# Kernel optimization log

Hardware: AMD Instinct MI355X
Metric: run time of the kernel (lower is better)

Reference implementation:

```python
import jax, jax.numpy as jnp
import numpy as np

S, L = 4096, 16          # words per sentence, max chars per word
V, DW, DC, H, T = 128000, 128, 64, 256, 50
CHAR_VOCAB = 53


def lstm_cell(h, c, x, Wih, Whh, bih, bhh):
    # PyTorch LSTM gate order: i, f, g, o
    g = x @ Wih.T + h @ Whh.T + bih + bhh
    i, f, gg, o = jnp.split(g, 4, axis=-1)
    c = jax.nn.sigmoid(f) * c + jax.nn.sigmoid(i) * jnp.tanh(gg)
    h = jax.nn.sigmoid(o) * jnp.tanh(c)
    return h, c


def setup_inputs() -> dict:
    key = jax.random.key(0)
    ks = jax.random.split(key, 14)
    s = 0.1
    return {
        "word_ids": jax.random.randint(ks[0], (S,), 0, V),
        "char_ids": jax.random.randint(ks[1], (S, L), 0, CHAR_VOCAB),
        "word_lengths": jax.random.randint(ks[2], (S,), 1, L + 1),
        "word_emb": jax.random.normal(ks[3], (V, DW), jnp.float32) * s,
        "char_emb": jax.random.normal(ks[4], (CHAR_VOCAB, DC), jnp.float32) * s,
        "c_Wih": jax.random.normal(ks[5], (4 * DC, DC), jnp.float32) * s,
        "c_Whh": jax.random.normal(ks[6], (4 * DC, DC), jnp.float32) * s,
        "c_bih": jnp.zeros((4 * DC,), jnp.float32),
        "c_bhh": jnp.zeros((4 * DC,), jnp.float32),
        "w_Wih": jax.random.normal(ks[7], (4 * H, DW + DC), jnp.float32) * s,
        "w_Whh": jax.random.normal(ks[8], (4 * H, H), jnp.float32) * s,
        "w_bih": jnp.zeros((4 * H,), jnp.float32),
        "w_bhh": jnp.zeros((4 * H,), jnp.float32),
        "out_W": jax.random.normal(ks[9], (T, H), jnp.float32) * s,
        "out_b": jnp.zeros((T,), jnp.float32),
    }


def reference(word_ids, char_ids, word_lengths, word_emb, char_emb,
              c_Wih, c_Whh, c_bih, c_bhh,
              w_Wih, w_Whh, w_bih, w_bhh, out_W, out_b):
    # --- char-level LSTM, all words batched together, masked for ragged lengths ---
    ce = char_emb[char_ids]                 # [S, L, DC]
    xs = jnp.swapaxes(ce, 0, 1)             # [L, S, DC]

    def char_step(carry, inp):
        h, c = carry
        x, t = inp
        hn, cn = lstm_cell(h, c, x, c_Wih, c_Whh, c_bih, c_bhh)
        valid = (t < word_lengths)[:, None]  # freeze state once past word length
        return (jnp.where(valid, hn, h), jnp.where(valid, cn, c)), None

    z = jnp.zeros((S, DC), ce.dtype)
    (h_char, _), _ = jax.lax.scan(char_step, (z, z), (xs, jnp.arange(L)))

    # --- word-level LSTM over the sentence (batch = 1, as in the original) ---
    we = word_emb[word_ids]                          # [S, DW]
    wx = jnp.concatenate([we, h_char], axis=-1)      # [S, DW+DC]

    def word_step(carry, x):
        h, c = lstm_cell(carry[0], carry[1], x, w_Wih, w_Whh, w_bih, w_bhh)
        return (h, c), h

    zh = jnp.zeros((H,), wx.dtype)
    _, hs = jax.lax.scan(word_step, (zh, zh), wx)    # hs: [S, H]

    logits = hs @ out_W.T + out_b                    # [S, T]
    return jax.nn.log_softmax(logits, axis=1)
```

## Files before the change

### kernel.cpp

```cpp
#include <hip/hip_runtime.h>
#include <hip/hip_bf16.h>
#include <math.h>

#define S   4096
#define L   16
#define DW  128
#define DC  64
#define HH  256
#define TT  50
#define KX  (DW + DC)
#define G4  (4 * HH)
#define CWPG 8
#define SB  16

typedef unsigned long long u64;

__device__ __forceinline__ float frcp(float x) { return __builtin_amdgcn_rcpf(x); }
__device__ __forceinline__ float fsigmoid(float x) { return frcp(1.f + __expf(-x)); }
__device__ __forceinline__ float ftanh(float x) {
    float ax = fabsf(x);
    float t  = __expf(-2.f * ax);
    float r  = (1.f - t) * frcp(1.f + t);
    return x < 0.f ? -r : r;
}

__device__ __forceinline__ void publish_h(u64* p, int tag, float v) {
    u64 pk = ((u64)(unsigned)tag << 32) | (u64)__float_as_uint(v);
    __hip_atomic_store(p, pk, __ATOMIC_RELAXED, __HIP_MEMORY_SCOPE_AGENT);
}
__device__ __forceinline__ float poll_h(const u64* p, int tag) {
    u64 v;
    do {
        v = __hip_atomic_load(p, __ATOMIC_RELAXED, __HIP_MEMORY_SCOPE_AGENT);
    } while ((int)(unsigned)(v >> 32) != tag);
    return __uint_as_float((unsigned)v);
}

__global__ __launch_bounds__(256) void char_lstm_kernel(
    const int* __restrict__ char_ids, const int* __restrict__ word_len,
    const float* __restrict__ char_emb,
    const float* __restrict__ cWih, const float* __restrict__ cWhh,
    const float* __restrict__ cbih, const float* __restrict__ cbhh,
    float* __restrict__ h_char)
{
    const int t = threadIdx.x;
    const int g = t >> 6;
    const int j = t & 63;
    const int r = g * 64 + j;

    float wih[64], whh[64];
#pragma unroll
    for (int k = 0; k < 64; ++k) wih[k] = cWih[r * 64 + k];
#pragma unroll
    for (int k = 0; k < 64; ++k) whh[k] = cWhh[r * 64 + k];
    const float cb = cbih[r] + cbhh[r];

    __shared__ float ce[L * 64];
    __shared__ float hbuf[64];
    __shared__ float gbuf[256];
    __shared__ int   ids[L];
    __shared__ int   wlen;

    const int w0 = blockIdx.x * CWPG;
    for (int wi = 0; wi < CWPG; ++wi) {
        const int w = w0 + wi;
        if (t < L)   ids[t] = char_ids[w * L + t];
        if (t == 64) wlen = word_len[w];
        if (t < 64)  hbuf[t] = 0.f;
        float c = 0.f;
        float hreg = 0.f;
        __syncthreads();
        for (int i = t; i < L * 64; i += 256)
            ce[i] = char_emb[ids[i >> 6] * 64 + (i & 63)];
        __syncthreads();

        for (int step = 0; step < L; ++step) {
            float acc = cb;
            const float* x = &ce[step * 64];
#pragma unroll
            for (int k = 0; k < 64; k += 4) {
                float4 xv = *(const float4*)&x[k];
                acc += wih[k] * xv.x + wih[k + 1] * xv.y + wih[k + 2] * xv.z + wih[k + 3] * xv.w;
            }
#pragma unroll
            for (int k = 0; k < 64; k += 4) {
                float4 hv = *(const float4*)&hbuf[k];
                acc += whh[k] * hv.x + whh[k + 1] * hv.y + whh[k + 2] * hv.z + whh[k + 3] * hv.w;
            }
            float a = (g == 2) ? ftanh(acc) : fsigmoid(acc);
            gbuf[r] = a;
            __syncthreads();
            if (g == 0) {
                if (step < wlen) {
                    float iv = gbuf[j], fv = gbuf[64 + j], gg = gbuf[128 + j], ov = gbuf[192 + j];
                    c = fv * c + iv * gg;
                    hreg = ov * ftanh(c);
                }
                hbuf[j] = hreg;
            }
            __syncthreads();
        }
        if (g == 0) h_char[w * 64 + j] = hreg;
        __syncthreads();
    }
}

__global__ void transpose_wih(const float* __restrict__ W, float* __restrict__ Wt)
{
    int idx = blockIdx.x * 256 + threadIdx.x;
    if (idx < KX * G4) {
        int r = idx & (G4 - 1);
        int k = idx >> 10;
        Wt[idx] = W[r * KX + k];
    }
}

__global__ __launch_bounds__(256) void xproj_kernel(
    const int* __restrict__ word_ids, const float* __restrict__ word_emb,
    const float* __restrict__ h_char, const float* __restrict__ Wt,
    const float* __restrict__ wbih, const float* __restrict__ wbhh,
    float* __restrict__ Xp)
{
    const int t = threadIdx.x;
    const int s0 = blockIdx.x * SB;
    __shared__ float xs[SB][KX];
    __shared__ int   wid[SB];
    if (t < SB) wid[t] = word_ids[s0 + t];
    __syncthreads();
    for (int i = t; i < SB * DW; i += 256) {
        int s = i >> 7, k = i & 127;
        xs[s][k] = word_emb[wid[s] * DW + k];
    }
    for (int i = t; i < SB * DC; i += 256) {
        int s = i >> 6, k = i & 63;
        xs[s][DW + k] = h_char[(s0 + s) * DC + k];
    }
    __syncthreads();

    float acc[4][SB];
#pragma unroll
    for (int c = 0; c < 4; ++c)
#pragma unroll
        for (int s = 0; s < SB; ++s) acc[c][s] = 0.f;

    for (int kk = 0; kk < KX; ++kk) {
        float w0v = Wt[kk * G4 + t];
        float w1v = Wt[kk * G4 + 256 + t];
        float w2v = Wt[kk * G4 + 512 + t];
        float w3v = Wt[kk * G4 + 768 + t];
#pragma unroll
        for (int s = 0; s < SB; ++s) {
            float xv = xs[s][kk];
            acc[0][s] += w0v * xv;
            acc[1][s] += w1v * xv;
            acc[2][s] += w2v * xv;
            acc[3][s] += w3v * xv;
        }
    }
#pragma unroll
    for (int c = 0; c < 4; ++c) {
        int r = c * 256 + t;
        float bb = wbih[r] + wbhh[r];
#pragma unroll
        for (int s = 0; s < SB; ++s) Xp[(s0 + s) * G4 + r] = acc[c][s] + bb;
    }
}

__global__ __launch_bounds__(1024) void word_lstm_kernel(
    const float* __restrict__ Xp, const float* __restrict__ Whh,
    u64* __restrict__ hs64, float* __restrict__ hs)
{
    const int b  = blockIdx.x;
    const int t  = threadIdx.x;
    const int rl = t >> 2;
    const int q  = t & 3;
    const int gt = rl >> 6;
    const int jj = rl & 63;
    const int r  = gt * 256 + b * 64 + jj;

    float w[64];
#pragma unroll
    for (int i = 0; i < 64; ++i)
        w[i] = Whh[r * 256 + q * 64 + i];

    float c = 0.f;

    __shared__ float h_lds[4 * 68];
    __shared__ float g_lds[256];

    for (int s = 0; s < S; ++s) {
        float xp = Xp[s * G4 + r];
        if (t < 256)
            h_lds[(t >> 6) * 68 + (t & 63)] = poll_h(&hs64[s * 256 + t], s);
        __syncthreads();

        float acc = 0.f;
        const float* hq = &h_lds[q * 68];
#pragma unroll
        for (int i4 = 0; i4 < 16; ++i4) {
            float4 hv = *(const float4*)&hq[4 * i4];
            acc += w[4 * i4] * hv.x + w[4 * i4 + 1] * hv.y +
                   w[4 * i4 + 2] * hv.z + w[4 * i4 + 3] * hv.w;
        }
        acc += __shfl_xor(acc, 1);
        acc += __shfl_xor(acc, 2);
        if (q == 0) {
            float gv = acc + xp;
            g_lds[rl] = (gt == 2) ? ftanh(gv) : fsigmoid(gv);
        }
        __syncthreads();
        if (t < 64) {
            float iv = g_lds[t], fv = g_lds[64 + t], gg = g_lds[128 + t], ov = g_lds[192 + t];
            c = fv * c + iv * gg;
            float h = ov * ftanh(c);
            publish_h(&hs64[(s + 1) * 256 + b * 64 + t], s + 1, h);
            hs[(s + 1) * HH + b * 64 + t] = h;
        }
        __syncthreads();
    }
}

__global__ __launch_bounds__(256) void out_proj_kernel(
    const float* __restrict__ hs, const float* __restrict__ outW,
    const float* __restrict__ outb, float* __restrict__ out)
{
    const int row  = blockIdx.x * 4 + (threadIdx.x >> 6);
    const int lane = threadIdx.x & 63;
    const float* h = hs + HH + row * HH;
    float logit = -1e30f;
    if (lane < TT) {
        const float* wr = outW + lane * HH;
        float a = outb[lane];
#pragma unroll 8
        for (int k = 0; k < HH; k += 4) {
            float4 hv = *(const float4*)&h[k];
            float4 wv = *(const float4*)&wr[k];
            a += hv.x * wv.x + hv.y * wv.y + hv.z * wv.z + hv.w * wv.w;
        }
        logit = a;
    }
    float mx = logit;
#pragma unroll
    for (int d = 32; d; d >>= 1) mx = fmaxf(mx, __shfl_xor(mx, d));
    float ex = (lane < TT) ? __expf(logit - mx) : 0.f;
    float sm = ex;
#pragma unroll
    for (int d = 32; d; d >>= 1) sm += __shfl_xor(sm, d);
    float ls = logit - mx - __logf(sm);
    if (lane < TT) out[row * TT + lane] = ls;
}

extern "C" void kernel_launch(void* const* d_in, const int* in_sizes, int n_in,
                              void* d_out, int out_size, void* d_ws, size_t ws_size,
                              hipStream_t stream)
{
    const int*   word_ids = (const int*)d_in[0];
    const int*   char_ids = (const int*)d_in[1];
    const int*   word_len = (const int*)d_in[2];
    const float* word_emb = (const float*)d_in[3];
    const float* char_emb = (const float*)d_in[4];
    const float* cWih     = (const float*)d_in[5];
    const float* cWhh     = (const float*)d_in[6];
    const float* cbih     = (const float*)d_in[7];
    const float* cbhh     = (const float*)d_in[8];
    const float* wWih     = (const float*)d_in[9];
    const float* wWhh     = (const float*)d_in[10];
    const float* wbih     = (const float*)d_in[11];
    const float* wbhh     = (const float*)d_in[12];
    const float* outW     = (const float*)d_in[13];
    const float* outb     = (const float*)d_in[14];
    float* out = (float*)d_out;

    float* h_char = (float*)d_ws;
    float* Wt     = h_char + 262144;
    float* Xp     = Wt + 196608;
    float* hs     = Xp + 4194304;
    u64*   hs64   = (u64*)(hs + 1048832);

    hipMemsetAsync(hs, 0, HH * sizeof(float), stream);
    hipMemsetAsync(hs64, 0, 256 * sizeof(u64), stream);

    hipLaunchKernelGGL(char_lstm_kernel, dim3(S / CWPG), dim3(256), 0, stream,
                       char_ids, word_len, char_emb, cWih, cWhh, cbih, cbhh, h_char);
    hipLaunchKernelGGL(transpose_wih, dim3((KX * G4 + 255) / 256), dim3(256), 0, stream,
                       wWih, Wt);
    hipLaunchKernelGGL(xproj_kernel, dim3(S / SB), dim3(256), 0, stream,
                       word_ids, word_emb, h_char, Wt, wbih, wbhh, Xp);
    hipLaunchKernelGGL(word_lstm_kernel, dim3(4), dim3(1024), 0, stream,
                       Xp, wWhh, hs64, hs);
    hipLaunchKernelGGL(out_proj_kernel, dim3(S / 4), dim3(256), 0, stream,
                       hs, outW, outb, out);
}
```

Before: 5.915 ms.

## Co-locate word-LSTM blocks on one XCD and exchange hidden state via L2

Launches 64 blocks and uses an XCC_ID-based election so the four working blocks all sit on the same XCD; the rest exit. Hidden-state exchange then uses non-coherent global stores and sc0 polling that stay within that XCD's L2, with an agent-scope fallback copy after a spin limit. It also double-buffers the LDS hidden vector, writes each block's own slice locally, and drops one __syncthreads per step. This targets the cross-XCD coherence latency on the serial 4096-step recurrence. The cost is extra launch blocks, a duplicate publish, and reliance on the XCD placement and cache behaviour.

```diff
diff --git a/kernel.cpp b/kernel.cpp
--- a/kernel.cpp
+++ b/kernel.cpp
@@ -12,6 +12,7 @@
 #define G4  (4 * HH)
 #define CWPG 8
 #define SB  16
+#define SPIN_MAX 16384
 
 typedef unsigned long long u64;
 
@@ -24,14 +25,23 @@
     return x < 0.f ? -r : r;
 }
 
-__device__ __forceinline__ void publish_h(u64* p, int tag, float v) {
-    u64 pk = ((u64)(unsigned)tag << 32) | (u64)__float_as_uint(v);
-    __hip_atomic_store(p, pk, __ATOMIC_RELAXED, __HIP_MEMORY_SCOPE_AGENT);
-}
-__device__ __forceinline__ float poll_h(const u64* p, int tag) {
+__device__ __forceinline__ void publish_l2(u64* p, u64 pk) {
+    asm volatile("global_store_dwordx2 %0, %1, off" :: "v"(p), "v"(pk) : "memory");
+}
+__device__ __forceinline__ float poll_h(const u64* pf, const u64* ps, int tag,
+                                        bool& mall) {
     u64 v;
+    if (!mall) {
+        int spins = 0;
+        for (;;) {
+            asm volatile("global_load_dwordx2 %0, %1, off sc0\n\ts_waitcnt vmcnt(0)"
+                         : "=v"(v) : "v"(pf) : "memory");
+            if ((int)(unsigned)(v >> 32) == tag) return __uint_as_float((unsigned)v);
+            if (++spins > SPIN_MAX) { mall = true; break; }
+        }
+    }
     do {
-        v = __hip_atomic_load(p, __ATOMIC_RELAXED, __HIP_MEMORY_SCOPE_AGENT);
+        v = __hip_atomic_load(ps, __ATOMIC_RELAXED, __HIP_MEMORY_SCOPE_AGENT);
     } while ((int)(unsigned)(v >> 32) != tag);
     return __uint_as_float((unsigned)v);
 }
@@ -168,10 +178,33 @@
 
 __global__ __launch_bounds__(1024) void word_lstm_kernel(
     const float* __restrict__ Xp, const float* __restrict__ Whh,
-    u64* __restrict__ hs64, float* __restrict__ hs)
-{
-    const int b  = blockIdx.x;
-    const int t  = threadIdx.x;
+    u64* __restrict__ hs64, u64* __restrict__ hs64m,
+    float* __restrict__ hs, int* __restrict__ ctrl)
+{
+    __shared__ int s_slot;
+    const int t = threadIdx.x;
+    if (t == 0) {
+        int xcd;
+        asm volatile("s_getreg_b32 %0, hwreg(HW_REG_XCC_ID, 0, 4)" : "=s"(xcd));
+        xcd &= 7;
+        int rank = __hip_atomic_fetch_add(&ctrl[xcd], 1, __ATOMIC_RELAXED,
+                                          __HIP_MEMORY_SCOPE_AGENT);
+        if (rank == 3) {
+            int exp = -1;
+            __hip_atomic_compare_exchange_strong(&ctrl[8], &exp, xcd,
+                __ATOMIC_RELAXED, __ATOMIC_RELAXED, __HIP_MEMORY_SCOPE_AGENT);
+        }
+        int chosen;
+        do {
+            chosen = __hip_atomic_load(&ctrl[8], __ATOMIC_RELAXED,
+                                       __HIP_MEMORY_SCOPE_AGENT);
+        } while (chosen == -1);
+        s_slot = (chosen == xcd && rank < 4) ? rank : -1;
+    }
+    __syncthreads();
+    const int b = s_slot;
+    if (b < 0) return;
+
     const int rl = t >> 2;
     const int q  = t & 3;
     const int gt = rl >> 6;
@@ -184,18 +217,23 @@
         w[i] = Whh[r * 256 + q * 64 + i];
 
     float c = 0.f;
-
-    __shared__ float h_lds[4 * 68];
+    bool mall = false;
+
+    __shared__ float h_lds[2][4 * 68];
     __shared__ float g_lds[256];
+
+    if (t < 64) h_lds[0][b * 68 + t] = 0.f;
 
     for (int s = 0; s < S; ++s) {
         float xp = Xp[s * G4 + r];
-        if (t < 256)
-            h_lds[(t >> 6) * 68 + (t & 63)] = poll_h(&hs64[s * 256 + t], s);
+        const int pb = s & 1;
+        if (t < 256 && (t >> 6) != b)
+            h_lds[pb][(t >> 6) * 68 + (t & 63)] =
+                poll_h(&hs64[s * 256 + t], &hs64m[s * 256 + t], s, mall);
         __syncthreads();
 
         float acc = 0.f;
-        const float* hq = &h_lds[q * 68];
+        const float* hq = &h_lds[pb][q * 68];
 #pragma unroll
         for (int i4 = 0; i4 < 16; ++i4) {
             float4 hv = *(const float4*)&hq[4 * i4];
@@ -213,10 +251,13 @@
             float iv = g_lds[t], fv = g_lds[64 + t], gg = g_lds[128 + t], ov = g_lds[192 + t];
             c = fv * c + iv * gg;
             float h = ov * ftanh(c);
-            publish_h(&hs64[(s + 1) * 256 + b * 64 + t], s + 1, h);
+            u64 pk = ((u64)(unsigned)(s + 1) << 32) | (u64)__float_as_uint(h);
+            publish_l2(&hs64[(s + 1) * 256 + b * 64 + t], pk);
+            __hip_atomic_store(&hs64m[(s + 1) * 256 + b * 64 + t], pk,
+                               __ATOMIC_RELAXED, __HIP_MEMORY_SCOPE_AGENT);
             hs[(s + 1) * HH + b * 64 + t] = h;
-        }
-        __syncthreads();
+            h_lds[(s + 1) & 1][b * 68 + t] = h;
+        }
     }
 }
 
@@ -276,9 +317,14 @@
     float* Xp     = Wt + 196608;
     float* hs     = Xp + 4194304;
     u64*   hs64   = (u64*)(hs + 1048832);
+    u64*   hs64m  = hs64 + 4097 * 256;
+    int*   ctrl   = (int*)(hs64m + 4097 * 256);
 
     hipMemsetAsync(hs, 0, HH * sizeof(float), stream);
     hipMemsetAsync(hs64, 0, 256 * sizeof(u64), stream);
+    hipMemsetAsync(hs64m, 0, 256 * sizeof(u64), stream);
+    hipMemsetAsync(ctrl, 0, 8 * sizeof(int), stream);
+    hipMemsetAsync(ctrl + 8, 0xFF, sizeof(int), stream);
 
     hipLaunchKernelGGL(char_lstm_kernel, dim3(S / CWPG), dim3(256), 0, stream,
                        char_ids, word_len, char_emb, cWih, cWhh, cbih, cbhh, h_char);
@@ -286,8 +332,8 @@
                        wWih, Wt);
     hipLaunchKernelGGL(xproj_kernel, dim3(S / SB), dim3(256), 0, stream,
                        word_ids, word_emb, h_char, Wt, wbih, wbhh, Xp);
-    hipLaunchKernelGGL(word_lstm_kernel, dim3(4), dim3(1024), 0, stream,
-                       Xp, wWhh, hs64, hs);
+    hipLaunchKernelGGL(word_lstm_kernel, dim3(64), dim3(1024), 0, stream,
+                       Xp, wWhh, hs64, hs64m, hs, ctrl);
     hipLaunchKernelGGL(out_proj_kernel, dim3(S / 4), dim3(256), 0, stream,
                        hs, outW, outb, out);
 }
```

Measured after the change: 11.19 ms. +89.2%, slower.
